# Kernel optimization log

Measured on AMD Instinct MI355X. Metric: run time of the kernel, lower is better.

The kernel has to match this reference:

```python
import jax, jax.numpy as jnp
import numpy as np

B, C, T, H, W = 4, 256, 64, 32, 32
K = 64  # kernel_size spans the whole sequence


def setup_inputs() -> dict:
    key = jax.random.key(0)
    kx, kw = jax.random.split(key)
    x = jax.random.normal(kx, (B, C, T, H, W), dtype=jnp.float32)
    # nn.Parameter(torch.randn(channels, 1, kernel_size) * 0.01)
    weight = jax.random.normal(kw, (C, 1, K), dtype=jnp.float32) * 0.01
    return {"x": x, "weight": weight}


def reference(x, weight):
    b, c, t, h, w = x.shape
    k = weight.shape[-1]
    pad = k - 1
    # torch .view: raw row-major reinterpretation of (B,C,T,H,W) as (B*H*W, C, T)
    x_ = x.reshape(b * h * w, c, t)
    # depthwise (groups=C) cross-correlation, symmetric padding like F.conv1d(padding=pad)
    y = jax.lax.conv_general_dilated(
        x_, weight,
        window_strides=(1,),
        padding=[(pad, pad)],
        feature_group_count=c,
        dimension_numbers=("NCH", "OIH", "NCH"),
    )  # (B*H*W, C, T + pad)
    y = y[:, :, -t:]  # causal slice: keep last T positions
    # .view(B,H,W,C,T).permute(0,3,4,1,2) -> (B,C,T,H,W)
    y = y.reshape(b, h, w, c, t).transpose(0, 3, 4, 1, 2)
    return y
```

## Files before the change

kernel.cpp:

```cpp
#include <hip/hip_runtime.h>


constexpr int Cc = 256;
constexpr int Tt = 64;
constexpr int Kk = 64;
constexpr int CT = Cc * Tt;
constexpr int NC_TILE = 4;
constexpr int NN_TILE = 64;
constexpr int CHUNK_BYTES = NC_TILE * Tt * 4;
constexpr int CHUNK_STRIDE = CHUNK_BYTES + 16;
constexpr int LDS_BYTES = NN_TILE * CHUNK_STRIDE;

__global__ __launch_bounds__(256, 2)
void DepthwiseTemporalConv_24962349924982_kernel(const float* __restrict__ x,
                                                 const float* __restrict__ w,
                                                 float* __restrict__ out) {
    __shared__ __align__(16) char lds[LDS_BYTES];
    const int tid  = threadIdx.x;
    const int lane = tid & 63;
    const int wv   = tid >> 6;

    const int n_tile = blockIdx.x & 63;
    const int c_tile = blockIdx.x >> 6;
    const int n0 = n_tile * NN_TILE;
    const int c0 = c_tile * NC_TILE;

    for (int it = 0; it < 16; ++it) {
        const int i = (it << 2) + wv;
        const float* gsrc = x + (size_t)(n0 + i) * CT + c0 * Tt + lane * 4;
        __builtin_amdgcn_global_load_lds(
            (const __attribute__((address_space(1))) void*)gsrc,
            (__attribute__((address_space(3))) void*)(lds + i * CHUNK_STRIDE),
            16, 0, 0);
    }

    float wr[Kk];
    {
        const float4* wp = (const float4*)(w + (size_t)(c0 + wv) * Kk);
        #pragma unroll
        for (int m = 0; m < 16; ++m) {
            const float4 v = wp[m];
            wr[4*m+0] = v.x; wr[4*m+1] = v.y; wr[4*m+2] = v.z; wr[4*m+3] = v.w;
        }
    }

    __syncthreads();

    float xr[Tt];
    {
        const char* base = lds + lane * CHUNK_STRIDE + wv * (Tt * 4);
        #pragma unroll
        for (int m = 0; m < 16; ++m) {
            const float4 v = *(const float4*)(base + m * 16);
            xr[4*m+0] = v.x; xr[4*m+1] = v.y; xr[4*m+2] = v.z; xr[4*m+3] = v.w;
        }
    }

    const int n = n0 + lane;
    const int c = c0 + wv;
    float* obase = out + (size_t)(n >> 10) * (Cc * Tt * 1024)
                       + (size_t)c * (Tt * 1024) + (n & 1023);
    #pragma unroll
    for (int t = 0; t < Tt; ++t) {
        const int len = Tt - t;
        float a0 = 0.f, a1 = 0.f;
        #pragma unroll
        for (int k = 0; k + 1 < len; k += 2) {
            a0 = fmaf(xr[t + k],     wr[k],     a0);
            a1 = fmaf(xr[t + k + 1], wr[k + 1], a1);
        }
        if (len & 1) a0 = fmaf(xr[Tt - 1], wr[len - 1], a0);
        obase[(size_t)t * 1024] = a0 + a1;
    }
}

extern "C" void kernel_launch(void* const* d_in, const int* in_sizes, int n_in,
                              void* d_out, int out_size, void* d_ws, size_t ws_size,
                              hipStream_t stream) {
    const float* x = (const float*)d_in[0];
    const float* w = (const float*)d_in[1];
    float* out = (float*)d_out;
    DepthwiseTemporalConv_24962349924982_kernel<<<dim3(4096), dim3(256), 0, stream>>>(x, w, out);
}
```

Before: 137.1 us.

## Load input rows directly into registers, drop LDS staging and barrier

```diff
diff --git a/kernel.cpp b/kernel.cpp
--- a/kernel.cpp
+++ b/kernel.cpp
@@ -5,63 +5,41 @@
 constexpr int Tt = 64;
 constexpr int Kk = 64;
 constexpr int CT = Cc * Tt;
-constexpr int NC_TILE = 4;
-constexpr int NN_TILE = 64;
-constexpr int CHUNK_BYTES = NC_TILE * Tt * 4;
-constexpr int CHUNK_STRIDE = CHUNK_BYTES + 16;
-constexpr int LDS_BYTES = NN_TILE * CHUNK_STRIDE;
 
-__global__ __launch_bounds__(256, 2)
+__global__ __launch_bounds__(256, 3)
 void DepthwiseTemporalConv_24962349924982_kernel(const float* __restrict__ x,
                                                  const float* __restrict__ w,
                                                  float* __restrict__ out) {
-    __shared__ __align__(16) char lds[LDS_BYTES];
     const int tid  = threadIdx.x;
     const int lane = tid & 63;
     const int wv   = tid >> 6;
 
     const int n_tile = blockIdx.x & 63;
     const int c_tile = blockIdx.x >> 6;
-    const int n0 = n_tile * NN_TILE;
-    const int c0 = c_tile * NC_TILE;
+    const int n  = n_tile * 64 + lane;
+    const int cv = c_tile * 4 + wv;
 
-    for (int it = 0; it < 16; ++it) {
-        const int i = (it << 2) + wv;
-        const float* gsrc = x + (size_t)(n0 + i) * CT + c0 * Tt + lane * 4;
-        __builtin_amdgcn_global_load_lds(
-            (const __attribute__((address_space(1))) void*)gsrc,
-            (__attribute__((address_space(3))) void*)(lds + i * CHUNK_STRIDE),
-            16, 0, 0);
+    const int cu = __builtin_amdgcn_readfirstlane(cv);
+    const float* __restrict__ wp = w + (size_t)cu * Kk;
+    float wr[Kk];
+    #pragma unroll
+    for (int m = 0; m < 16; ++m) {
+        const float4 v = *(const float4*)(wp + 4 * m);
+        wr[4*m+0] = v.x; wr[4*m+1] = v.y; wr[4*m+2] = v.z; wr[4*m+3] = v.w;
     }
 
-    float wr[Kk];
-    {
-        const float4* wp = (const float4*)(w + (size_t)(c0 + wv) * Kk);
-        #pragma unroll
-        for (int m = 0; m < 16; ++m) {
-            const float4 v = wp[m];
-            wr[4*m+0] = v.x; wr[4*m+1] = v.y; wr[4*m+2] = v.z; wr[4*m+3] = v.w;
-        }
+    float xr[Tt];
+    const float* __restrict__ rowp = x + (size_t)n * CT + (size_t)cu * Tt;
+    #pragma unroll
+    for (int m = 15; m >= 0; --m) {
+        const float4 v = *(const float4*)(rowp + 4 * m);
+        xr[4*m+0] = v.x; xr[4*m+1] = v.y; xr[4*m+2] = v.z; xr[4*m+3] = v.w;
     }
 
-    __syncthreads();
-
-    float xr[Tt];
-    {
-        const char* base = lds + lane * CHUNK_STRIDE + wv * (Tt * 4);
-        #pragma unroll
-        for (int m = 0; m < 16; ++m) {
-            const float4 v = *(const float4*)(base + m * 16);
-            xr[4*m+0] = v.x; xr[4*m+1] = v.y; xr[4*m+2] = v.z; xr[4*m+3] = v.w;
-        }
-    }
-
-    const int n = n0 + lane;
-    const int c = c0 + wv;
-    float* obase = out + (size_t)(n >> 10) * (Cc * Tt * 1024)
-                       + (size_t)c * (Tt * 1024) + (n & 1023);
+    float* __restrict__ obase = out + (size_t)(n >> 10) * (Cc * Tt * 1024)
+                                    + (size_t)cv * (Tt * 1024) + (n & 1023);
     #pragma unroll
-    for (int t = 0; t < Tt; ++t) {
+    for (int t = Tt - 1; t >= 0; --t) {
         const int len = Tt - t;
         float a0 = 0.f, a1 = 0.f;
         #pragma unroll
```

Measured after the change: 155.2 us. 1.13x slower.

## Use single-wave blocks per channel and replace block barrier with waitcnt

Applied to the files above, without the earlier changes.

```diff
diff --git a/kernel.cpp b/kernel.cpp
--- a/kernel.cpp
+++ b/kernel.cpp
@@ -5,29 +5,25 @@
 constexpr int Tt = 64;
 constexpr int Kk = 64;
 constexpr int CT = Cc * Tt;
-constexpr int NC_TILE = 4;
-constexpr int NN_TILE = 64;
-constexpr int CHUNK_BYTES = NC_TILE * Tt * 4;
-constexpr int CHUNK_STRIDE = CHUNK_BYTES + 16;
-constexpr int LDS_BYTES = NN_TILE * CHUNK_STRIDE;
+constexpr int CHUNK_STRIDE = 1024 + 16;
+constexpr int LDS_BYTES = 16 * CHUNK_STRIDE;
 
-__global__ __launch_bounds__(256, 2)
+__global__ __launch_bounds__(64, 2)
 void DepthwiseTemporalConv_24962349924982_kernel(const float* __restrict__ x,
                                                  const float* __restrict__ w,
                                                  float* __restrict__ out) {
     __shared__ __align__(16) char lds[LDS_BYTES];
-    const int tid  = threadIdx.x;
-    const int lane = tid & 63;
-    const int wv   = tid >> 6;
+    const int lane = threadIdx.x & 63;
 
     const int n_tile = blockIdx.x & 63;
-    const int c_tile = blockIdx.x >> 6;
-    const int n0 = n_tile * NN_TILE;
-    const int c0 = c_tile * NC_TILE;
+    const int c      = blockIdx.x >> 6;
+    const int n0 = n_tile * 64;
+    const int n  = n0 + lane;
 
-    for (int it = 0; it < 16; ++it) {
-        const int i = (it << 2) + wv;
-        const float* gsrc = x + (size_t)(n0 + i) * CT + c0 * Tt + lane * 4;
+    #pragma unroll
+    for (int i = 0; i < 16; ++i) {
+        const float* gsrc = x + (size_t)(n0 + 4 * i + (lane >> 4)) * CT
+                              + (size_t)c * Tt + (lane & 15) * 4;
         __builtin_amdgcn_global_load_lds(
             (const __attribute__((address_space(1))) void*)gsrc,
             (__attribute__((address_space(3))) void*)(lds + i * CHUNK_STRIDE),
@@ -36,7 +32,7 @@
 
     float wr[Kk];
     {
-        const float4* wp = (const float4*)(w + (size_t)(c0 + wv) * Kk);
+        const float4* wp = (const float4*)(w + (size_t)c * Kk);
         #pragma unroll
         for (int m = 0; m < 16; ++m) {
             const float4 v = wp[m];
@@ -44,11 +40,12 @@
         }
     }
 
-    __syncthreads();
+    asm volatile("s_waitcnt vmcnt(0)" ::: "memory");
+    __builtin_amdgcn_sched_barrier(0);
 
     float xr[Tt];
     {
-        const char* base = lds + lane * CHUNK_STRIDE + wv * (Tt * 4);
+        const char* base = lds + (lane >> 2) * CHUNK_STRIDE + (lane & 3) * 256;
         #pragma unroll
         for (int m = 0; m < 16; ++m) {
             const float4 v = *(const float4*)(base + m * 16);
@@ -56,10 +53,8 @@
         }
     }
 
-    const int n = n0 + lane;
-    const int c = c0 + wv;
-    float* obase = out + (size_t)(n >> 10) * (Cc * Tt * 1024)
-                       + (size_t)c * (Tt * 1024) + (n & 1023);
+    float* __restrict__ obase = out + (size_t)(n >> 10) * (Cc * Tt * 1024)
+                                    + (size_t)c * (Tt * 1024) + (n & 1023);
     #pragma unroll
     for (int t = 0; t < Tt; ++t) {
         const int len = Tt - t;
@@ -80,5 +75,5 @@
     const float* x = (const float*)d_in[0];
     const float* w = (const float*)d_in[1];
     float* out = (float*)d_out;
-    DepthwiseTemporalConv_24962349924982_kernel<<<dim3(4096), dim3(256), 0, stream>>>(x, w, out);
+    DepthwiseTemporalConv_24962349924982_kernel<<<dim3(16384), dim3(64), 0, stream>>>(x, w, out);
 }
```

Result: slower. 147.9 us (+7.8%).
